# Performance work log

Measured on AMD Instinct MI355X. Metric: run time of the kernel, lower is better.

Reference implementation:

```python
import jax, jax.numpy as jnp
import numpy as np

EPS = 1e-5

def _ln(x, g, b):
    m = jnp.mean(x, axis=-1, keepdims=True)
    v = jnp.var(x, axis=-1, keepdims=True)
    return (x - m) * jax.lax.rsqrt(v + EPS) * g + b

def _lrelu(x):
    return jnp.where(x >= 0, x, 0.2 * x)

def _xavier(k, shape):
    a = (6.0 / (shape[0] + shape[1])) ** 0.5
    return jax.random.uniform(k, shape, minval=-a, maxval=a, dtype=jnp.float32)

def setup_inputs() -> dict:
    key = jax.random.key(0)
    ks = jax.random.split(key, 10)
    B, P, I = 32, 2048, 4096          # batch, n_pathway, n_img_features
    HQ, QK, HV, L = 64, 64, 64, 256   # hidden_dim_q(==qk), hidden_dim_qk, hidden_dim_v, classifier latent
    return {
        "img": jax.random.normal(ks[0], (B, 4, I), jnp.float32),
        "pathway": jax.random.normal(ks[1], (B, P), jnp.float32),
        "qw": _xavier(ks[2], (1, HQ)),
        "qw2": _xavier(ks[3], (HQ, QK)),
        "kw": _xavier(ks[4], (4, QK)),
        "vw": _xavier(ks[5], (4, HV)),
        "vw2": jax.random.normal(ks[6], (HV, 1), jnp.float32) * (HV ** -0.5),
        "q_g": jnp.ones(QK, jnp.float32), "q_b": jnp.zeros(QK, jnp.float32),
        "k_g": jnp.ones(QK, jnp.float32), "k_b": jnp.zeros(QK, jnp.float32),
        "v_g": jnp.ones(HV, jnp.float32), "v_b": jnp.zeros(HV, jnp.float32),
        "n1_g": jnp.ones(P, jnp.float32), "n1_b": jnp.zeros(P, jnp.float32),
        "n2_g": jnp.ones(L, jnp.float32), "n2_b": jnp.zeros(L, jnp.float32),
        "w1": _xavier(ks[7], (L, P)), "b1": jnp.zeros(L, jnp.float32),
        "w2": jax.random.normal(ks[8], (1, L), jnp.float32) * (L ** -0.5),
        "b2": jnp.zeros(1, jnp.float32),
    }

def reference(img, pathway, qw, qw2, kw, vw, vw2,
              q_g, q_b, k_g, k_b, v_g, v_b, n1_g, n1_b, n2_g, n2_b,
              w1, b1, w2, b2):
    P = pathway.shape[1]
    vrf = (P ** 0.5) / 2.0            # gamma * sqrt(n_pathway) / 2, gamma=1.0
    C = 0.5                           # soft_sign_constant
    img_t = jnp.swapaxes(img, -2, -1)              # [B, I, 4]
    # query path: outer product with [1, HQ] weight, LN, leaky, second proj, leaky (source applies key_relu to query)
    qm = pathway[..., None] @ qw                   # [B, P, HQ]
    qm = _lrelu(_ln(qm, q_g, q_b))
    qm = _lrelu(qm @ qw2)                          # [B, P, QK]
    # key path: LN only (source never relu's the key matrix)
    km = _ln(img_t @ kw, k_g, k_b)                 # [B, I, QK]
    # value path
    vm = _lrelu(_ln(img_t @ vw, v_g, v_b)) @ vw2   # [B, I, 1]
    # relu + variance-scale + soft-sign attention
    attn = jnp.einsum('bpd,bid->bpi', qm, km)      # [B, P, I]
    attn = jax.nn.relu(attn) / vrf
    attn = attn / (jnp.abs(attn) + C)
    out = attn @ vm                                # [B, P, 1]
    # classifier head (dropout = identity in eval)
    h = _lrelu(_ln(out[..., 0], n1_g, n1_b))       # [B, P]
    h = _lrelu(_ln(h @ w1.T + b1, n2_g, n2_b))     # [B, L]
    logits = h @ w2.T + b2                         # [B, 1]
    return (logits, attn, out)
```

## Files before the change

### kernel.cpp

```cpp
#include <hip/hip_runtime.h>
#include <hip/hip_bf16.h>

#define EPS 1e-5f
#define INV_VRF 4.4194173824159220e-02f

#define NB 32
#define NP 2048
#define NI 4096
#define ND 64
#define NL 256

#define ATTN_OFF 32L
#define OUT_OFF  268435488L

typedef __attribute__((ext_vector_type(4))) float vf4;
typedef __attribute__((ext_vector_type(8))) short vs8;

__device__ __forceinline__ unsigned short f2bf(float f) {
  unsigned int u = __float_as_uint(f);
  unsigned int r = (u + 0x7FFFu + ((u >> 16) & 1u)) >> 16;
  return (unsigned short)r;
}

__device__ __forceinline__ int kperm(int d) {
  int dd = d & 31;
  return (d & 32) + (((dd & 15) >> 2) << 3) + ((dd >> 4) << 2) + (dd & 3);
}

__global__ __launch_bounds__(256) void k_qm(
    const float* __restrict__ pathway, const float* __restrict__ qw,
    const float* __restrict__ qw2, const float* __restrict__ q_g,
    const float* __restrict__ q_b, unsigned short* __restrict__ qm)
{
  __shared__ float qw2s[64 * 64];
  int tid = threadIdx.x, lane = tid & 63, w = tid >> 6;
  for (int idx = tid; idx < 4096; idx += 256) qw2s[idx] = qw2[idx];
  float qwv = qw[lane], qg = q_g[lane], qb = q_b[lane];
  float s1 = qwv, s2 = qwv * qwv;
  #pragma unroll
  for (int m = 32; m; m >>= 1) { s1 += __shfl_xor(s1, m); s2 += __shfl_xor(s2, m); }
  float mq = s1 * (1.f / 64.f), vq = s2 * (1.f / 64.f) - mq * mq;
  float qc = qwv - mq;
  int pdst = kperm(lane);
  __syncthreads();
  long base = (long)blockIdx.x * 32 + w * 8;
  for (int r = 0; r < 8; ++r) {
    long row = base + r;
    float s = pathway[row];
    float alpha = s * rsqrtf(s * s * vq + EPS);
    float t = alpha * qc * qg + qb;
    t = t >= 0.f ? t : 0.2f * t;
    float acc = 0.f;
    #pragma unroll
    for (int h = 0; h < 64; ++h) acc += __shfl(t, h) * qw2s[h * 64 + lane];
    acc = acc >= 0.f ? acc : 0.2f * acc;
    qm[row * 64 + pdst] = f2bf(acc);
  }
}

__global__ __launch_bounds__(256) void k_kmvm(
    const float* __restrict__ img, const float* __restrict__ kw,
    const float* __restrict__ vw, const float* __restrict__ vw2,
    const float* __restrict__ k_g, const float* __restrict__ k_b,
    const float* __restrict__ v_g, const float* __restrict__ v_b,
    unsigned short* __restrict__ km, float* __restrict__ vm)
{
  int tid = threadIdx.x, lane = tid & 63, w = tid >> 6;
  long row = (long)blockIdx.x * 4 + w;
  int b = (int)(row >> 12), i = (int)(row & 4095);
  const float* ib = img + (long)b * 4 * 4096 + i;
  float xv = (lane < 4) ? ib[lane * 4096] : 0.f;
  float x0 = __shfl(xv, 0), x1 = __shfl(xv, 1), x2 = __shfl(xv, 2), x3 = __shfl(xv, 3);
  int d = lane;
  float kp = x0 * kw[d] + x1 * kw[64 + d] + x2 * kw[128 + d] + x3 * kw[192 + d];
  float vp = x0 * vw[d] + x1 * vw[64 + d] + x2 * vw[128 + d] + x3 * vw[192 + d];
  float a1 = kp, a2 = kp * kp, a3 = vp, a4 = vp * vp;
  #pragma unroll
  for (int m = 32; m; m >>= 1) {
    a1 += __shfl_xor(a1, m); a2 += __shfl_xor(a2, m);
    a3 += __shfl_xor(a3, m); a4 += __shfl_xor(a4, m);
  }
  float mk = a1 * (1.f / 64.f), vk = a2 * (1.f / 64.f) - mk * mk;
  float mv = a3 * (1.f / 64.f), vv = a4 * (1.f / 64.f) - mv * mv;
  float kmv = (kp - mk) * rsqrtf(vk + EPS) * k_g[d] + k_b[d];
  km[row * 64 + kperm(d)] = f2bf(kmv);
  float y = (vp - mv) * rsqrtf(vv + EPS) * v_g[d] + v_b[d];
  y = y >= 0.f ? y : 0.2f * y;
  float pv = y * vw2[d];
  #pragma unroll
  for (int m = 32; m; m >>= 1) pv += __shfl_xor(pv, m);
  if (lane == 0) vm[row] = pv;
}

__global__ __launch_bounds__(256) void k_attn(
    const unsigned short* __restrict__ qm, const unsigned short* __restrict__ km,
    const float* __restrict__ vm, float* __restrict__ dout)
{
  __shared__ __align__(16) float tr_s[4][16 * 128];
  int tid = threadIdx.x, lane = tid & 63, w = tid >> 6;
  int g = lane >> 4, c = lane & 15;
  int bid = blockIdx.x;
  int lbid = (bid & 7) * 128 + (bid >> 3);
  int b = lbid >> 5, pt = lbid & 31;
  long p_base = (long)b * NP + pt * 64;
  int prow = w * 16;

  const unsigned short* qrow = qm + (p_base + prow + c) * 64;
  vs8 afr0 = *(const vs8*)(qrow + g * 8);
  vs8 afr1 = *(const vs8*)(qrow + 32 + g * 8);

  const unsigned short* kb = km + (long)b * NI * 64;
  const float* vmb = vm + (long)b * NI;
  float* trw = tr_s[w];
  float* outbase = dout + ATTN_OFF + (p_base + prow) * (long)NI;
  float oacc[4] = {0.f, 0.f, 0.f, 0.f};

  for (int s = 0; s < 32; ++s) {
    int i0 = s * 128;
    vf4 acc[8];
    #pragma unroll
    for (int nt = 0; nt < 8; ++nt) acc[nt] = (vf4){0.f, 0.f, 0.f, 0.f};
    #pragma unroll
    for (int nt = 0; nt < 8; ++nt) {
      const unsigned short* krow = kb + (long)(i0 + nt * 16 + c) * 64;
      vs8 b0 = *(const vs8*)(krow + g * 8);
      vs8 b1 = *(const vs8*)(krow + 32 + g * 8);
      acc[nt] = __builtin_amdgcn_mfma_f32_16x16x32_bf16(afr0, b0, acc[nt], 0, 0, 0);
      acc[nt] = __builtin_amdgcn_mfma_f32_16x16x32_bf16(afr1, b1, acc[nt], 0, 0, 0);
    }
    #pragma unroll
    for (int nt = 0; nt < 8; ++nt) {
      #pragma unroll
      for (int r = 0; r < 4; ++r) {
        float x = fmaxf(acc[nt][r], 0.f) * INV_VRF;
        float y = x * __builtin_amdgcn_rcpf(x + 0.5f);
        int row = g * 4 + r;
        int f4 = (nt * 4 + (c >> 2)) ^ row;
        trw[row * 128 + f4 * 4 + (c & 3)] = y;
      }
    }
    #pragma unroll
    for (int pass = 0; pass < 2; ++pass) {
      vf4 vmv = *(const vf4*)(vmb + i0 + pass * 64 + c * 4);
      #pragma unroll
      for (int j = 0; j < 4; ++j) {
        int row = j * 4 + g;
        int f4 = (pass * 16 + c) ^ row;
        vf4 yv = *(const vf4*)&trw[row * 128 + f4 * 4];
        __builtin_nontemporal_store(
            yv, (vf4*)(outbase + (long)row * NI + i0 + pass * 64 + c * 4));
        oacc[j] += yv[0] * vmv[0] + yv[1] * vmv[1] + yv[2] * vmv[2] + yv[3] * vmv[3];
      }
    }
  }
  #pragma unroll
  for (int m = 1; m <= 8; m <<= 1) {
    #pragma unroll
    for (int j = 0; j < 4; ++j) oacc[j] += __shfl_xor(oacc[j], m);
  }
  if (c == 0) {
    #pragma unroll
    for (int j = 0; j < 4; ++j)
      dout[OUT_OFF + p_base + prow + j * 4 + g] = oacc[j];
  }
}

__global__ __launch_bounds__(256) void k_head(
    const float* __restrict__ n1_g, const float* __restrict__ n1_b,
    const float* __restrict__ n2_g, const float* __restrict__ n2_b,
    const float* __restrict__ w1, const float* __restrict__ b1,
    const float* __restrict__ w2, const float* __restrict__ b2,
    float* __restrict__ dout)
{
  int tid = threadIdx.x, lane = tid & 63, w = tid >> 6;
  int b = blockIdx.x;
  __shared__ float h1s[2048];
  __shared__ float red[8];
  const float* orow = dout + OUT_OFF + (long)b * NP;
  float vals[8];
  float s1 = 0.f, s2 = 0.f;
  #pragma unroll
  for (int j = 0; j < 8; ++j) {
    float v = orow[j * 256 + tid];
    vals[j] = v; s1 += v; s2 += v * v;
  }
  #pragma unroll
  for (int m = 32; m; m >>= 1) { s1 += __shfl_xor(s1, m); s2 += __shfl_xor(s2, m); }
  if (lane == 0) { red[w] = s1; red[4 + w] = s2; }
  __syncthreads();
  float S1 = red[0] + red[1] + red[2] + red[3];
  float S2 = red[4] + red[5] + red[6] + red[7];
  float mean = S1 * (1.f / 2048.f);
  float var = S2 * (1.f / 2048.f) - mean * mean;
  float rs = rsqrtf(var + EPS);
  __syncthreads();
  #pragma unroll
  for (int j = 0; j < 8; ++j) {
    int p = j * 256 + tid;
    float h = (vals[j] - mean) * rs * n1_g[p] + n1_b[p];
    h = h >= 0.f ? h : 0.2f * h;
    h1s[p] = h;
  }
  __syncthreads();
  float acc = b1[tid];
  const float* wr = w1 + (long)tid * 2048;
  for (int qq = 0; qq < 2048; qq += 4) {
    float4 wv = *(const float4*)(wr + qq);
    acc += wv.x * h1s[qq] + wv.y * h1s[qq + 1] + wv.z * h1s[qq + 2] + wv.w * h1s[qq + 3];
  }
  float t1 = acc, t2 = acc * acc;
  #pragma unroll
  for (int m = 32; m; m >>= 1) { t1 += __shfl_xor(t1, m); t2 += __shfl_xor(t2, m); }
  if (lane == 0) { red[w] = t1; red[4 + w] = t2; }
  __syncthreads();
  float T1 = red[0] + red[1] + red[2] + red[3];
  float T2 = red[4] + red[5] + red[6] + red[7];
  float m2 = T1 * (1.f / 256.f);
  float v2 = T2 * (1.f / 256.f) - m2 * m2;
  float rs2 = rsqrtf(v2 + EPS);
  float h2 = (acc - m2) * rs2 * n2_g[tid] + n2_b[tid];
  h2 = h2 >= 0.f ? h2 : 0.2f * h2;
  float lg = h2 * w2[tid];
  #pragma unroll
  for (int m = 32; m; m >>= 1) lg += __shfl_xor(lg, m);
  __syncthreads();
  if (lane == 0) red[w] = lg;
  __syncthreads();
  if (tid == 0) dout[b] = red[0] + red[1] + red[2] + red[3] + b2[0];
}

extern "C" void kernel_launch(void* const* d_in, const int* in_sizes, int n_in,
                              void* d_out, int out_size, void* d_ws, size_t ws_size,
                              hipStream_t stream)
{
  const float* img     = (const float*)d_in[0];
  const float* pathway = (const float*)d_in[1];
  const float* qw      = (const float*)d_in[2];
  const float* qw2     = (const float*)d_in[3];
  const float* kw      = (const float*)d_in[4];
  const float* vw      = (const float*)d_in[5];
  const float* vw2     = (const float*)d_in[6];
  const float* q_g     = (const float*)d_in[7];
  const float* q_b     = (const float*)d_in[8];
  const float* k_g     = (const float*)d_in[9];
  const float* k_b     = (const float*)d_in[10];
  const float* v_g     = (const float*)d_in[11];
  const float* v_b     = (const float*)d_in[12];
  const float* n1_g    = (const float*)d_in[13];
  const float* n1_b    = (const float*)d_in[14];
  const float* n2_g    = (const float*)d_in[15];
  const float* n2_b    = (const float*)d_in[16];
  const float* w1      = (const float*)d_in[17];
  const float* b1      = (const float*)d_in[18];
  const float* w2      = (const float*)d_in[19];
  const float* b2      = (const float*)d_in[20];
  float* dout = (float*)d_out;

  unsigned short* qm_ws = (unsigned short*)d_ws;
  unsigned short* km_ws = (unsigned short*)((char*)d_ws + 8388608);
  float*          vm_ws = (float*)((char*)d_ws + 25165824);

  k_qm<<<dim3(2048), dim3(256), 0, stream>>>(pathway, qw, qw2, q_g, q_b, qm_ws);
  k_kmvm<<<dim3(32768), dim3(256), 0, stream>>>(img, kw, vw, vw2, k_g, k_b, v_g, v_b, km_ws, vm_ws);
  k_attn<<<dim3(1024), dim3(256), 0, stream>>>(qm_ws, km_ws, vm_ws, dout);
  k_head<<<dim3(32), dim3(256), 0, stream>>>(n1_g, n1_b, n2_g, n2_b, w1, b1, w2, b2, dout);
}
```

Baseline: 432.5 us.

## Warp-specialize attention kernel into MFMA producer and store consumer waves

Splits the attention block into four compute waves and four store waves. The compute waves run the MFMA, apply the soft-sign and write tiles into a double-buffered LDS area. The store waves stream the previous tile to global memory with nontemporal stores, with barriers between phases, so compute and the large attn writeback overlap. The out accumulation now uses the register values directly instead of rereading LDS. This adds a block-wide barrier every phase and doubles LDS use, which may reduce occupancy.

```diff
diff --git a/kernel.cpp b/kernel.cpp
--- a/kernel.cpp
+++ b/kernel.cpp
@@ -92,76 +92,91 @@
   if (lane == 0) vm[row] = pv;
 }
 
-__global__ __launch_bounds__(256) void k_attn(
+__global__ __launch_bounds__(512) void k_attn(
     const unsigned short* __restrict__ qm, const unsigned short* __restrict__ km,
     const float* __restrict__ vm, float* __restrict__ dout)
 {
-  __shared__ __align__(16) float tr_s[4][16 * 128];
+  __shared__ __align__(16) float buf[2][4][16 * 128];
   int tid = threadIdx.x, lane = tid & 63, w = tid >> 6;
   int g = lane >> 4, c = lane & 15;
   int bid = blockIdx.x;
   int lbid = (bid & 7) * 128 + (bid >> 3);
   int b = lbid >> 5, pt = lbid & 31;
   long p_base = (long)b * NP + pt * 64;
-  int prow = w * 16;
-
-  const unsigned short* qrow = qm + (p_base + prow + c) * 64;
-  vs8 afr0 = *(const vs8*)(qrow + g * 8);
-  vs8 afr1 = *(const vs8*)(qrow + 32 + g * 8);
-
-  const unsigned short* kb = km + (long)b * NI * 64;
-  const float* vmb = vm + (long)b * NI;
-  float* trw = tr_s[w];
-  float* outbase = dout + ATTN_OFF + (p_base + prow) * (long)NI;
-  float oacc[4] = {0.f, 0.f, 0.f, 0.f};
-
-  for (int s = 0; s < 32; ++s) {
-    int i0 = s * 128;
-    vf4 acc[8];
+
+  if (w < 4) {
+    int prow = w * 16;
+    const unsigned short* qrow = qm + (p_base + prow + c) * 64;
+    vs8 afr0 = *(const vs8*)(qrow + g * 8);
+    vs8 afr1 = *(const vs8*)(qrow + 32 + g * 8);
+    const unsigned short* kb = km + (long)b * NI * 64;
+    const float* vmb = vm + (long)b * NI;
+    float oacc[4] = {0.f, 0.f, 0.f, 0.f};
+
+    for (int ph = 0; ph < 33; ++ph) {
+      if (ph < 32) {
+        int i0 = ph * 128;
+        float* trw = buf[ph & 1][w];
+        vf4 acc[8];
+        #pragma unroll
+        for (int nt = 0; nt < 8; ++nt) acc[nt] = (vf4){0.f, 0.f, 0.f, 0.f};
+        #pragma unroll
+        for (int nt = 0; nt < 8; ++nt) {
+          const unsigned short* krow = kb + (long)(i0 + nt * 16 + c) * 64;
+          vs8 b0 = *(const vs8*)(krow + g * 8);
+          vs8 b1 = *(const vs8*)(krow + 32 + g * 8);
+          acc[nt] = __builtin_amdgcn_mfma_f32_16x16x32_bf16(afr0, b0, acc[nt], 0, 0, 0);
+          acc[nt] = __builtin_amdgcn_mfma_f32_16x16x32_bf16(afr1, b1, acc[nt], 0, 0, 0);
+        }
+        #pragma unroll
+        for (int nt = 0; nt < 8; ++nt) {
+          float vmv = vmb[i0 + nt * 16 + c];
+          #pragma unroll
+          for (int r = 0; r < 4; ++r) {
+            float x = fmaxf(acc[nt][r], 0.f) * INV_VRF;
+            float y = x * __builtin_amdgcn_rcpf(x + 0.5f);
+            int row = g * 4 + r;
+            int f4 = (nt * 4 + (c >> 2)) ^ row;
+            trw[row * 128 + f4 * 4 + (c & 3)] = y;
+            oacc[r] += y * vmv;
+          }
+        }
+      }
+      asm volatile("s_waitcnt lgkmcnt(0)" ::: "memory");
+      __builtin_amdgcn_s_barrier();
+    }
     #pragma unroll
-    for (int nt = 0; nt < 8; ++nt) acc[nt] = (vf4){0.f, 0.f, 0.f, 0.f};
-    #pragma unroll
-    for (int nt = 0; nt < 8; ++nt) {
-      const unsigned short* krow = kb + (long)(i0 + nt * 16 + c) * 64;
-      vs8 b0 = *(const vs8*)(krow + g * 8);
-      vs8 b1 = *(const vs8*)(krow + 32 + g * 8);
-      acc[nt] = __builtin_amdgcn_mfma_f32_16x16x32_bf16(afr0, b0, acc[nt], 0, 0, 0);
-      acc[nt] = __builtin_amdgcn_mfma_f32_16x16x32_bf16(afr1, b1, acc[nt], 0, 0, 0);
-    }
-    #pragma unroll
-    for (int nt = 0; nt < 8; ++nt) {
+    for (int m = 1; m <= 8; m <<= 1) {
       #pragma unroll
-      for (int r = 0; r < 4; ++r) {
-        float x = fmaxf(acc[nt][r], 0.f) * INV_VRF;
-        float y = x * __builtin_amdgcn_rcpf(x + 0.5f);
-        int row = g * 4 + r;
-        int f4 = (nt * 4 + (c >> 2)) ^ row;
-        trw[row * 128 + f4 * 4 + (c & 3)] = y;
+      for (int r = 0; r < 4; ++r) oacc[r] += __shfl_xor(oacc[r], m);
+    }
+    if (c == 0) {
+      #pragma unroll
+      for (int r = 0; r < 4; ++r)
+        dout[OUT_OFF + p_base + prow + g * 4 + r] = oacc[r];
+    }
+  } else {
+    int cw = w - 4, prow = cw * 16;
+    float* outbase = dout + ATTN_OFF + (p_base + prow) * (long)NI;
+    for (int ph = 0; ph < 33; ++ph) {
+      if (ph >= 1) {
+        int s = ph - 1, i0 = s * 128;
+        const float* trw = buf[s & 1][cw];
+        #pragma unroll
+        for (int pass = 0; pass < 2; ++pass) {
+          #pragma unroll
+          for (int j = 0; j < 4; ++j) {
+            int row = j * 4 + g;
+            int f4 = (pass * 16 + c) ^ row;
+            vf4 yv = *(const vf4*)&trw[row * 128 + f4 * 4];
+            __builtin_nontemporal_store(
+                yv, (vf4*)(outbase + (long)row * NI + i0 + pass * 64 + c * 4));
+          }
+        }
       }
-    }
-    #pragma unroll
-    for (int pass = 0; pass < 2; ++pass) {
-      vf4 vmv = *(const vf4*)(vmb + i0 + pass * 64 + c * 4);
-      #pragma unroll
-      for (int j = 0; j < 4; ++j) {
-        int row = j * 4 + g;
-        int f4 = (pass * 16 + c) ^ row;
-        vf4 yv = *(const vf4*)&trw[row * 128 + f4 * 4];
-        __builtin_nontemporal_store(
-            yv, (vf4*)(outbase + (long)row * NI + i0 + pass * 64 + c * 4));
-        oacc[j] += yv[0] * vmv[0] + yv[1] * vmv[1] + yv[2] * vmv[2] + yv[3] * vmv[3];
-      }
-    }
-  }
-  #pragma unroll
-  for (int m = 1; m <= 8; m <<= 1) {
-    #pragma unroll
-    for (int j = 0; j < 4; ++j) oacc[j] += __shfl_xor(oacc[j], m);
-  }
-  if (c == 0) {
-    #pragma unroll
-    for (int j = 0; j < 4; ++j)
-      dout[OUT_OFF + p_base + prow + j * 4 + g] = oacc[j];
+      asm volatile("s_waitcnt lgkmcnt(0)" ::: "memory");
+      __builtin_amdgcn_s_barrier();
+    }
   }
 }
 
@@ -262,6 +277,6 @@
 
   k_qm<<<dim3(2048), dim3(256), 0, stream>>>(pathway, qw, qw2, q_g, q_b, qm_ws);
   k_kmvm<<<dim3(32768), dim3(256), 0, stream>>>(img, kw, vw, vw2, k_g, k_b, v_g, v_b, km_ws, vm_ws);
-  k_attn<<<dim3(1024), dim3(256), 0, stream>>>(qm_ws, km_ws, vm_ws, dout);
+  k_attn<<<dim3(1024), dim3(512), 0, stream>>>(qm_ws, km_ws, vm_ws, dout);
   k_head<<<dim3(32), dim3(256), 0, stream>>>(n1_g, n1_b, n2_g, n2_b, w1, b1, w2, b2, dout);
 }
```

Result: slower. 545.2 us (+26.1%).
